# Optimization experiments

Hardware: AMD Instinct MI355X
Metric: run time of the kernel (lower is better)

The kernel has to match this reference:

```python
import jax, jax.numpy as jnp
import numpy as np

IN_DIM = 256
OUT_DIM = 256
EMBED_DIM = 256
GROUPS = 8
BN_EPS = 1e-5


def conv2d(x, w, b, pad, groups=1):
    # x: NCHW, w: OIHW (I = in_ch / groups)
    out = jax.lax.conv_general_dilated(
        x, w, window_strides=(1, 1), padding=[(pad, pad), (pad, pad)],
        dimension_numbers=('NCHW', 'OIHW', 'NCHW'), feature_group_count=groups)
    return out + b[None, :, None, None]


def setup_inputs() -> dict:
    key = jax.random.key(0)
    ks = jax.random.split(key, 8)
    s = 0.05
    d = {}
    d['x'] = jax.random.normal(ks[0], (2, IN_DIM, 16, 16), jnp.float32)
    d['y'] = jax.random.normal(ks[1], (2, OUT_DIM, 128, 128), jnp.float32)
    # channle_reduce: Conv2d(256, 64, k=3, groups=64) -> weight (64, 4, 3, 3)
    d['w_cr'] = jax.random.normal(ks[2], (IN_DIM // 4, 4, 3, 3), jnp.float32) * s
    d['b_cr'] = jnp.zeros((IN_DIM // 4,), jnp.float32)
    # depthwise convs on 64 channels
    d['w_dw3'] = jax.random.normal(ks[3], (IN_DIM // 4, 1, 3, 3), jnp.float32) * s
    d['b_dw3'] = jnp.zeros((IN_DIM // 4,), jnp.float32)
    d['w_dw7'] = jax.random.normal(ks[4], (IN_DIM // 4, 1, 5, 5), jnp.float32) * s
    d['b_dw7'] = jnp.zeros((IN_DIM // 4,), jnp.float32)
    # gate: Conv2d(256, 128, 1) + BN + StarReLU
    d['w_gate'] = jax.random.normal(ks[5], (IN_DIM // 2, IN_DIM, 1, 1), jnp.float32) * s
    d['b_gate'] = jnp.zeros((IN_DIM // 2,), jnp.float32)
    d['bn_gamma'] = jnp.ones((IN_DIM // 2,), jnp.float32)
    d['bn_beta'] = jnp.zeros((IN_DIM // 2,), jnp.float32)
    d['bn_mean'] = jnp.zeros((IN_DIM // 2,), jnp.float32)
    d['bn_var'] = jnp.ones((IN_DIM // 2,), jnp.float32)
    d['sr_scale'] = jnp.ones((1,), jnp.float32)
    d['sr_bias'] = jnp.zeros((1,), jnp.float32)
    # linear1: Linear(16, 8192) -> torch weight shape (8192, 16)
    d['w_lin'] = jax.random.normal(ks[6], (OUT_DIM * EMBED_DIM // GROUPS, IN_DIM // (2 * GROUPS)), jnp.float32) * s
    d['b_lin'] = jnp.zeros((OUT_DIM * EMBED_DIM // GROUPS,), jnp.float32)
    return d


def reference(x, y, w_cr, b_cr, w_dw3, b_dw3, w_dw7, b_dw7, w_gate, b_gate,
              bn_gamma, bn_beta, bn_mean, bn_var, sr_scale, sr_bias, w_lin, b_lin):
    B, C, H, Wd = x.shape
    # gate branch: 1x1 conv -> BN (inference stats) -> StarReLU
    g = conv2d(x, w_gate, b_gate, 0)
    inv = (bn_gamma / jnp.sqrt(bn_var + BN_EPS))[None, :, None, None]
    g = (g - bn_mean[None, :, None, None]) * inv + bn_beta[None, :, None, None]
    g = sr_scale * jnp.square(jnp.maximum(g, 0.0)) + sr_bias
    # feature branch
    xr = conv2d(x, w_cr, b_cr, 1, groups=IN_DIM // 4)        # (B, 64, H, W)
    x3 = conv2d(xr, w_dw3, b_dw3, 1, groups=IN_DIM // 4)
    x7 = conv2d(xr, w_dw7, b_dw7, 2, groups=IN_DIM // 4)
    xc = jnp.concatenate([x3, x7], axis=1) * g               # (B, 128, H, W)
    # per-pixel weight generation: (B,H,W,G,16) @ (16,8192)
    xc = xc.reshape(B, GROUPS, -1, H, Wd).transpose(0, 3, 4, 1, 2)
    wdec = jnp.einsum('bhwgi,oi->bhwgo', xc, w_lin) + b_lin  # (B,H,W,8,8192)
    # flatten (G, out*embed/G) -> (embed, out); matches torch reshape order
    wdec = wdec.reshape(B, H, Wd, EMBED_DIM, OUT_DIM)
    # patch-wise dynamic 1x1 conv == per-patch batched matmul
    b, c, h, w = y.shape
    fh, fw = H, Wd
    ph, pw = h // fh, w // fw
    yp = y.reshape(b, c, fh, ph, fw, pw)
    # out[b,e,f,p,g,q] = sum_c wdec[b,f,g,e,c] * y[b,c,f,p,g,q]
    out = jnp.einsum('bfgec,bcfpgq->befpgq', wdec, yp)
    return out.reshape(b, EMBED_DIM, h, w)
```

## Files before the change

kernel.cpp:

```cpp
#include <hip/hip_runtime.h>
#include <stdint.h>


typedef __attribute__((ext_vector_type(8))) short short8;
typedef __attribute__((ext_vector_type(4))) float f32x4;

#define BN_EPS 1e-5f

__device__ __forceinline__ unsigned short f2bf(float f) {
  unsigned u = __float_as_uint(f);
  return (unsigned short)((u + 0x8000u) >> 16);
}
__device__ __forceinline__ unsigned pk2bf(float a, float b) {
  unsigned ua = __float_as_uint(a), ub = __float_as_uint(b);
  return ((ua + 0x8000u) >> 16) | ((ub + 0x8000u) & 0xFFFF0000u);
}

__global__ __launch_bounds__(256) void k1a_groupconv(
    const float* __restrict__ x, const float* __restrict__ w_cr,
    const float* __restrict__ b_cr, float* __restrict__ xr)
{
  __shared__ float xs[4][256];
  int b = blockIdx.x >> 6, cr = blockIdx.x & 63;
  int t = threadIdx.x;
  {
    int ch = t >> 6, off = (t & 63) * 4;
    float4 v = *(const float4*)(x + b * 65536 + (cr * 4 + ch) * 256 + off);
    *(float4*)&xs[ch][off] = v;
  }
  __syncthreads();
  int h = t >> 4, w = t & 15;
  float a = b_cr[cr];
  #pragma unroll
  for (int ii = 0; ii < 4; ++ii) {
    const float* wp = w_cr + (cr * 4 + ii) * 9;
    #pragma unroll
    for (int ky = 0; ky < 3; ++ky) {
      int gy = h + ky - 1;
      #pragma unroll
      for (int kx = 0; kx < 3; ++kx) {
        int gx = w + kx - 1;
        float v = (gy >= 0 && gy < 16 && gx >= 0 && gx < 16) ? xs[ii][gy * 16 + gx] : 0.f;
        a += wp[ky * 3 + kx] * v;
      }
    }
  }
  xr[(b * 64 + cr) * 256 + t] = a;
}

__global__ __launch_bounds__(256) void k1b_gate_dw(
    const float* __restrict__ x, const float* __restrict__ xr,
    const float* __restrict__ w_dw3, const float* __restrict__ b_dw3,
    const float* __restrict__ w_dw7, const float* __restrict__ b_dw7,
    const float* __restrict__ w_gate, const float* __restrict__ b_gate,
    const float* __restrict__ bn_gamma, const float* __restrict__ bn_beta,
    const float* __restrict__ bn_mean, const float* __restrict__ bn_var,
    const float* __restrict__ sr_scale, const float* __restrict__ sr_bias,
    const float* __restrict__ w_lin, short* __restrict__ wlin_bf, short* __restrict__ xc_bf)
{
  __shared__ float xcen[256];
  __shared__ float gs[128];
  int blk = blockIdx.x;
  int b = blk >> 8, h = (blk >> 4) & 15, w = blk & 15;
  int t = threadIdx.x;

  { int idx = blk * 256 + t; wlin_bf[idx] = (short)f2bf(w_lin[idx]); }

  xcen[t] = x[b * 65536 + t * 256 + h * 16 + w];
  __syncthreads();

  int o = t >> 1, half = t & 1;
  {
    const float* wrow = w_gate + o * 256 + half * 128;
    const float* xcn  = xcen + half * 128;
    float ga = 0.f;
    #pragma unroll 8
    for (int ci = 0; ci < 128; ci += 4) {
      float4 wv = *(const float4*)(wrow + ci);
      float4 xv = *(const float4*)(xcn + ci);
      ga += wv.x * xv.x + wv.y * xv.y + wv.z * xv.z + wv.w * xv.w;
    }
    ga += __shfl_xor(ga, 1);
    float inv = bn_gamma[o] * rsqrtf(bn_var[o] + BN_EPS);
    float gg = (ga + b_gate[o] - bn_mean[o]) * inv + bn_beta[o];
    gg = fmaxf(gg, 0.f);
    gg = sr_scale[0] * gg * gg + sr_bias[0];
    if (half == 0) gs[o] = gg;
  }
  __syncthreads();

  if (t < 128) {
    int oc = t;
    float f0;
    if (oc < 64) {
      f0 = b_dw3[oc];
      const float* wp = w_dw3 + oc * 9;
      const float* xp = xr + (b * 64 + oc) * 256;
      #pragma unroll
      for (int ky = 0; ky < 3; ++ky) {
        int gy = h + ky - 1;
        #pragma unroll
        for (int kx = 0; kx < 3; ++kx) {
          int gx = w + kx - 1;
          float v = (gy >= 0 && gy < 16 && gx >= 0 && gx < 16) ? xp[gy * 16 + gx] : 0.f;
          f0 += wp[ky * 3 + kx] * v;
        }
      }
    } else {
      int c5 = oc - 64;
      f0 = b_dw7[c5];
      const float* wp = w_dw7 + c5 * 25;
      const float* xp = xr + (b * 64 + c5) * 256;
      #pragma unroll
      for (int ky = 0; ky < 5; ++ky) {
        int gy = h + ky - 2;
        #pragma unroll
        for (int kx = 0; kx < 5; ++kx) {
          int gx = w + kx - 2;
          float v = (gy >= 0 && gy < 16 && gx >= 0 && gx < 16) ? xp[gy * 16 + gx] : 0.f;
          f0 += wp[ky * 5 + kx] * v;
        }
      }
    }
    int pix = (b * 16 + h) * 16 + w;
    xc_bf[pix * 128 + oc] = (short)f2bf(f0 * gs[oc]);
  }
}

__global__ __launch_bounds__(256) void k2a_wgen(
    const short* __restrict__ wlin_bf, const short* __restrict__ xc_bf,
    const float* __restrict__ b_lin, short* __restrict__ wd)
{
  __shared__ __align__(16) short Wt[16 * 2048];
  int blk = blockIdx.x;
  int n0 = (blk >> 2) * 16;
  int oc = (blk & 3) * 2048;
  int tid = threadIdx.x;
  int wave = tid >> 6, lane = tid & 63;
  int quad = lane >> 4, l16 = lane & 15;

  short8 af = {0, 0, 0, 0, 0, 0, 0, 0};
  if (quad < 2) af = *(const short8*)(xc_bf + (n0 + l16) * 16 + quad * 8);

  f32x4 zero4 = {0.f, 0.f, 0.f, 0.f};
  #pragma unroll 8
  for (int i = 0; i < 32; ++i) {
    int o0 = wave * 512 + i * 16;
    short8 bf = {0, 0, 0, 0, 0, 0, 0, 0};
    if (quad < 2) bf = *(const short8*)(wlin_bf + (oc + o0 + l16) * 16 + quad * 8);
    f32x4 d = __builtin_amdgcn_mfma_f32_16x16x32_bf16(af, bf, zero4, 0, 0, 0);
    float bl = b_lin[oc + o0 + l16];
    #pragma unroll
    for (int r = 0; r < 4; ++r)
      Wt[(quad * 4 + r) * 2048 + o0 + l16] = (short)f2bf(d[r] + bl);
  }
  __syncthreads();

  const uint2* src = (const uint2*)Wt;
  #pragma unroll 8
  for (int j = 0; j < 32; ++j) {
    int fl = j * 256 + tid;
    int row = fl >> 9;
    int col = (fl & 511) * 4;
    *(uint2*)(wd + (size_t)(n0 + row) * 8192 + oc + col) = src[fl];
  }
}

__global__ __launch_bounds__(512, 6) void k2b_dynconv(
    const float* __restrict__ y, const short* __restrict__ wd,
    float* __restrict__ out)
{
  __shared__ __align__(16) short Ylds[8192];
  __shared__ __align__(16) float scratch[4096];

  int phys = blockIdx.x;
  int x_ = phys & 7, q_ = phys >> 3;
  int sub = q_ & 3, pphi = q_ >> 2;
  int pp = pphi * 8 + x_;
  int b = pp >> 7, f = (pp >> 3) & 15, gp = pp & 7;
  int g = gp * 2 + (sub & 1);
  int half = sub >> 1;

  int tid = threadIdx.x;
  int wave = tid >> 6, lane = tid & 63;
  int quad = lane >> 4, l16 = lane & 15;

  const float* yb = y + b * 4194304 + (f * 8 + half * 4) * 128 + g * 8;
  const short* wdp = wd + (size_t)(((b * 16 + f) * 16 + g)) * 65536;

  for (int pass = 0; pass < 2; ++pass) {
    #pragma unroll
    for (int it = 0; it < 2; ++it) {
      int task = it * 512 + tid;
      int c = task >> 3, pf = task & 7;
      float4 v = *(const float4*)(yb + (pass * 128 + c) * 16384 + (pf >> 1) * 128 + (pf & 3 & 1) * 4);
      *(float4*)&scratch[c * 32 + pf * 4] = v;
    }
    __syncthreads();
    {
      int pix = tid & 31, cg = tid >> 5;
      float s0 = scratch[(cg * 8 + 0) * 32 + pix];
      float s1 = scratch[(cg * 8 + 1) * 32 + pix];
      float s2 = scratch[(cg * 8 + 2) * 32 + pix];
      float s3 = scratch[(cg * 8 + 3) * 32 + pix];
      float s4 = scratch[(cg * 8 + 4) * 32 + pix];
      float s5 = scratch[(cg * 8 + 5) * 32 + pix];
      float s6 = scratch[(cg * 8 + 6) * 32 + pix];
      float s7 = scratch[(cg * 8 + 7) * 32 + pix];
      uint4 pk;
      pk.x = pk2bf(s0, s1); pk.y = pk2bf(s2, s3);
      pk.z = pk2bf(s4, s5); pk.w = pk2bf(s6, s7);
      int chunk = pass * 16 + cg;
      int physc = chunk ^ (pix & 7);
      *(uint4*)&Ylds[pix * 256 + physc * 8] = pk;
    }
    __syncthreads();
  }

  f32x4 acc[2][2];
  f32x4 zero4 = {0.f, 0.f, 0.f, 0.f};
  #pragma unroll
  for (int et = 0; et < 2; ++et)
    #pragma unroll
    for (int nt = 0; nt < 2; ++nt)
      acc[et][nt] = zero4;

  #pragma unroll 2
  for (int cc = 0; cc < 8; ++cc) {
    short8 A[2], Bf[2];
    #pragma unroll
    for (int et = 0; et < 2; ++et) {
      int e = wave * 32 + et * 16 + l16;
      A[et] = *(const short8*)(wdp + e * 256 + cc * 32 + quad * 8);
    }
    int chunk = cc * 4 + quad;
    #pragma unroll
    for (int nt = 0; nt < 2; ++nt) {
      int nn = nt * 16 + l16;
      int physc = chunk ^ (nn & 7);
      Bf[nt] = *(const short8*)&Ylds[nn * 256 + physc * 8];
    }
    #pragma unroll
    for (int et = 0; et < 2; ++et)
      #pragma unroll
      for (int nt = 0; nt < 2; ++nt)
        acc[et][nt] = __builtin_amdgcn_mfma_f32_16x16x32_bf16(A[et], Bf[nt], acc[et][nt], 0, 0, 0);
  }

  float* ob = out + b * 4194304 + (f * 8 + half * 4) * 128 + g * 8;
  #pragma unroll
  for (int et = 0; et < 2; ++et) {
    int e0 = wave * 32 + et * 16 + quad * 4;
    #pragma unroll
    for (int nt = 0; nt < 2; ++nt) {
      int pix = nt * 16 + l16;
      float* oa = ob + (pix >> 3) * 128 + (pix & 7);
      #pragma unroll
      for (int r = 0; r < 4; ++r)
        oa[(e0 + r) * 16384] = acc[et][nt][r];
    }
  }
}

extern "C" void kernel_launch(void* const* d_in, const int* in_sizes, int n_in,
                              void* d_out, int out_size, void* d_ws, size_t ws_size,
                              hipStream_t stream) {
  const float* x        = (const float*)d_in[0];
  const float* y        = (const float*)d_in[1];
  const float* w_cr     = (const float*)d_in[2];
  const float* b_cr     = (const float*)d_in[3];
  const float* w_dw3    = (const float*)d_in[4];
  const float* b_dw3    = (const float*)d_in[5];
  const float* w_dw7    = (const float*)d_in[6];
  const float* b_dw7    = (const float*)d_in[7];
  const float* w_gate   = (const float*)d_in[8];
  const float* b_gate   = (const float*)d_in[9];
  const float* bn_gamma = (const float*)d_in[10];
  const float* bn_beta  = (const float*)d_in[11];
  const float* bn_mean  = (const float*)d_in[12];
  const float* bn_var   = (const float*)d_in[13];
  const float* sr_scale = (const float*)d_in[14];
  const float* sr_bias  = (const float*)d_in[15];
  const float* w_lin    = (const float*)d_in[16];
  const float* b_lin    = (const float*)d_in[17];
  float* out = (float*)d_out;

  short* xc_bf   = (short*)d_ws;
  short* wlin_bf = (short*)((char*)d_ws + 131072);
  float* xr      = (float*)((char*)d_ws + 131072 + 262144);
  short* wd      = (short*)((char*)d_ws + 131072 + 262144 + 131072);

  hipLaunchKernelGGL(k1a_groupconv, dim3(128), dim3(256), 0, stream, x, w_cr, b_cr, xr);
  hipLaunchKernelGGL(k1b_gate_dw, dim3(512), dim3(256), 0, stream,
                     x, xr, w_dw3, b_dw3, w_dw7, b_dw7, w_gate, b_gate,
                     bn_gamma, bn_beta, bn_mean, bn_var, sr_scale, sr_bias,
                     w_lin, wlin_bf, xc_bf);
  hipLaunchKernelGGL(k2a_wgen, dim3(1024), dim3(256), 0, stream,
                     wlin_bf, xc_bf, b_lin, wd);
  hipLaunchKernelGGL(k2b_dynconv, dim3(1024), dim3(512), 0, stream, y, wd, out);
}
```

Baseline: 180.6 us.

## Fuse weight generation into dynamic conv by reassociating the per-pixel matmul

Removes the kernel that materializes the 64 MB-scale bf16 per-pixel weight tensor and instead computes W_lin^T·Y first, then contracts with the 16-wide xc vector plus a bias term via a second small MFMA. w_lin is transposed to bf16 and b_lin converted in the first kernel. This eliminates the large global write and read of generated weights at the cost of more MFMA work per block (wlinT re-read from L2 per block) and an extra bf16 rounding of the intermediate.

```diff
diff --git a/kernel.cpp b/kernel.cpp
--- a/kernel.cpp
+++ b/kernel.cpp
@@ -56,7 +56,8 @@
     const float* __restrict__ bn_gamma, const float* __restrict__ bn_beta,
     const float* __restrict__ bn_mean, const float* __restrict__ bn_var,
     const float* __restrict__ sr_scale, const float* __restrict__ sr_bias,
-    const float* __restrict__ w_lin, short* __restrict__ wlin_bf, short* __restrict__ xc_bf)
+    const float* __restrict__ w_lin, const float* __restrict__ b_lin,
+    short* __restrict__ wlinT, short* __restrict__ blin_bf, short* __restrict__ xc_bf)
 {
   __shared__ float xcen[256];
   __shared__ float gs[128];
@@ -64,7 +65,14 @@
   int b = blk >> 8, h = (blk >> 4) & 15, w = blk & 15;
   int t = threadIdx.x;
 
-  { int idx = blk * 256 + t; wlin_bf[idx] = (short)f2bf(w_lin[idx]); }
+  {
+    int idx = blk * 256 + t;
+    wlinT[(idx & 15) * 8192 + (idx >> 4)] = (short)f2bf(w_lin[idx]);
+  }
+  if (blk < 32) {
+    int idx = blk * 256 + t;
+    blin_bf[idx] = (short)f2bf(b_lin[idx]);
+  }
 
   xcen[t] = x[b * 65536 + t * 256 + h * 16 + w];
   __syncthreads();
@@ -127,47 +135,9 @@
   }
 }
 
-__global__ __launch_bounds__(256) void k2a_wgen(
-    const short* __restrict__ wlin_bf, const short* __restrict__ xc_bf,
-    const float* __restrict__ b_lin, short* __restrict__ wd)
-{
-  __shared__ __align__(16) short Wt[16 * 2048];
-  int blk = blockIdx.x;
-  int n0 = (blk >> 2) * 16;
-  int oc = (blk & 3) * 2048;
-  int tid = threadIdx.x;
-  int wave = tid >> 6, lane = tid & 63;
-  int quad = lane >> 4, l16 = lane & 15;
-
-  short8 af = {0, 0, 0, 0, 0, 0, 0, 0};
-  if (quad < 2) af = *(const short8*)(xc_bf + (n0 + l16) * 16 + quad * 8);
-
-  f32x4 zero4 = {0.f, 0.f, 0.f, 0.f};
-  #pragma unroll 8
-  for (int i = 0; i < 32; ++i) {
-    int o0 = wave * 512 + i * 16;
-    short8 bf = {0, 0, 0, 0, 0, 0, 0, 0};
-    if (quad < 2) bf = *(const short8*)(wlin_bf + (oc + o0 + l16) * 16 + quad * 8);
-    f32x4 d = __builtin_amdgcn_mfma_f32_16x16x32_bf16(af, bf, zero4, 0, 0, 0);
-    float bl = b_lin[oc + o0 + l16];
-    #pragma unroll
-    for (int r = 0; r < 4; ++r)
-      Wt[(quad * 4 + r) * 2048 + o0 + l16] = (short)f2bf(d[r] + bl);
-  }
-  __syncthreads();
-
-  const uint2* src = (const uint2*)Wt;
-  #pragma unroll 8
-  for (int j = 0; j < 32; ++j) {
-    int fl = j * 256 + tid;
-    int row = fl >> 9;
-    int col = (fl & 511) * 4;
-    *(uint2*)(wd + (size_t)(n0 + row) * 8192 + oc + col) = src[fl];
-  }
-}
-
-__global__ __launch_bounds__(512, 6) void k2b_dynconv(
-    const float* __restrict__ y, const short* __restrict__ wd,
+__global__ __launch_bounds__(256, 4) void k2_fused(
+    const float* __restrict__ y, const short* __restrict__ wlinT,
+    const short* __restrict__ blin, const short* __restrict__ xc_bf,
     float* __restrict__ out)
 {
   __shared__ __align__(16) short Ylds[8192];
@@ -184,21 +154,24 @@
   int tid = threadIdx.x;
   int wave = tid >> 6, lane = tid & 63;
   int quad = lane >> 4, l16 = lane & 15;
+  int pt = wave & 1, jh = wave >> 1;
+  int npix = (b * 16 + f) * 16 + g;
 
   const float* yb = y + b * 4194304 + (f * 8 + half * 4) * 128 + g * 8;
-  const short* wdp = wd + (size_t)(((b * 16 + f) * 16 + g)) * 65536;
 
   for (int pass = 0; pass < 2; ++pass) {
     #pragma unroll
+    for (int it = 0; it < 4; ++it) {
+      int task = it * 256 + tid;
+      int c = task >> 3, pf = task & 7;
+      *(float4*)&scratch[c * 32 + pf * 4] =
+          *(const float4*)(yb + (pass * 128 + c) * 16384 + (pf >> 1) * 128 + (pf & 1) * 4);
+    }
+    __syncthreads();
+    #pragma unroll
     for (int it = 0; it < 2; ++it) {
-      int task = it * 512 + tid;
-      int c = task >> 3, pf = task & 7;
-      float4 v = *(const float4*)(yb + (pass * 128 + c) * 16384 + (pf >> 1) * 128 + (pf & 3 & 1) * 4);
-      *(float4*)&scratch[c * 32 + pf * 4] = v;
-    }
-    __syncthreads();
-    {
-      int pix = tid & 31, cg = tid >> 5;
+      int task = it * 256 + tid;
+      int pix = task & 31, cg = task >> 5;
       float s0 = scratch[(cg * 8 + 0) * 32 + pix];
       float s1 = scratch[(cg * 8 + 1) * 32 + pix];
       float s2 = scratch[(cg * 8 + 2) * 32 + pix];
@@ -211,53 +184,72 @@
       pk.x = pk2bf(s0, s1); pk.y = pk2bf(s2, s3);
       pk.z = pk2bf(s4, s5); pk.w = pk2bf(s6, s7);
       int chunk = pass * 16 + cg;
-      int physc = chunk ^ (pix & 7);
-      *(uint4*)&Ylds[pix * 256 + physc * 8] = pk;
+      int ph = chunk ^ (pix & 7);
+      *(uint4*)&Ylds[pix * 256 + ph * 8] = pk;
     }
     __syncthreads();
   }
 
-  f32x4 acc[2][2];
+  short8 Bh[8];
+  int nn = pt * 16 + l16;
+  #pragma unroll
+  for (int kc = 0; kc < 8; ++kc) {
+    int chunk = kc * 4 + quad;
+    int ph = chunk ^ (nn & 7);
+    Bh[kc] = *(const short8*)&Ylds[nn * 256 + ph * 8];
+  }
+
+  short* tw = (short*)scratch + wave * 1024;
   f32x4 zero4 = {0.f, 0.f, 0.f, 0.f};
-  #pragma unroll
-  for (int et = 0; et < 2; ++et)
-    #pragma unroll
-    for (int nt = 0; nt < 2; ++nt)
-      acc[et][nt] = zero4;
+
+  {
+    f32x4 du = zero4;
+    #pragma unroll
+    for (int kc = 0; kc < 8; ++kc) {
+      short8 ab = *(const short8*)(blin + (jh * 16 + l16) * 256 + kc * 32 + quad * 8);
+      du = __builtin_amdgcn_mfma_f32_16x16x32_bf16(ab, Bh[kc], du, 0, 0, 0);
+    }
+    uint2 pk; pk.x = pk2bf(du[0], du[1]); pk.y = pk2bf(du[2], du[3]);
+    *(uint2*)&tw[512 + l16 * 16 + quad * 4] = pk;
+  }
+
+  short8 a2 = {0, 0, 0, 0, 0, 0, 0, 0};
+  if (quad < 2) {
+    if (l16 < 8) a2 = *(const short8*)(xc_bf + npix * 128 + l16 * 16 + quad * 8);
+  } else if (quad == 2) {
+    a2[0] = (short)0x3F80;
+  }
+
+  float* ob = out + b * 4194304 + (f * 8 + half * 4) * 128 + g * 8;
+  int pix = pt * 16 + l16;
+  float* oa = ob + (pix >> 3) * 128 + (pix & 7);
 
   #pragma unroll 2
-  for (int cc = 0; cc < 8; ++cc) {
-    short8 A[2], Bf[2];
-    #pragma unroll
-    for (int et = 0; et < 2; ++et) {
-      int e = wave * 32 + et * 16 + l16;
-      A[et] = *(const short8*)(wdp + e * 256 + cc * 32 + quad * 8);
-    }
-    int chunk = cc * 4 + quad;
-    #pragma unroll
-    for (int nt = 0; nt < 2; ++nt) {
-      int nn = nt * 16 + l16;
-      int physc = chunk ^ (nn & 7);
-      Bf[nt] = *(const short8*)&Ylds[nn * 256 + physc * 8];
-    }
-    #pragma unroll
-    for (int et = 0; et < 2; ++et)
-      #pragma unroll
-      for (int nt = 0; nt < 2; ++nt)
-        acc[et][nt] = __builtin_amdgcn_mfma_f32_16x16x32_bf16(A[et], Bf[nt], acc[et][nt], 0, 0, 0);
-  }
-
-  float* ob = out + b * 4194304 + (f * 8 + half * 4) * 128 + g * 8;
-  #pragma unroll
-  for (int et = 0; et < 2; ++et) {
-    int e0 = wave * 32 + et * 16 + quad * 4;
-    #pragma unroll
-    for (int nt = 0; nt < 2; ++nt) {
-      int pix = nt * 16 + l16;
-      float* oa = ob + (pix >> 3) * 128 + (pix & 7);
+  for (int j = 0; j < 16; ++j) {
+    int jg = jh * 16 + j;
+    const short* ap = wlinT + l16 * 8192 + jg * 256 + quad * 8;
+    f32x4 d = zero4;
+    #pragma unroll
+    for (int kc = 0; kc < 8; ++kc) {
+      short8 af = *(const short8*)(ap + kc * 32);
+      d = __builtin_amdgcn_mfma_f32_16x16x32_bf16(af, Bh[kc], d, 0, 0, 0);
+    }
+    short* tb = tw + (j & 1) * 256;
+    {
+      uint2 pk; pk.x = pk2bf(d[0], d[1]); pk.y = pk2bf(d[2], d[3]);
+      *(uint2*)&tb[l16 * 16 + quad * 4] = pk;
+    }
+    short8 b2 = {0, 0, 0, 0, 0, 0, 0, 0};
+    if (quad < 2) {
+      b2 = *(const short8*)&tb[l16 * 16 + quad * 8];
+    } else if (quad == 2) {
+      b2[0] = tw[512 + l16 * 16 + j];
+    }
+    f32x4 d2 = __builtin_amdgcn_mfma_f32_16x16x32_bf16(a2, b2, zero4, 0, 0, 0);
+    if (quad < 2) {
       #pragma unroll
       for (int r = 0; r < 4; ++r)
-        oa[(e0 + r) * 16384] = acc[et][nt][r];
+        oa[(size_t)((quad * 4 + r) * 32 + jg) * 16384] = d2[r];
     }
   }
 }
@@ -286,16 +278,15 @@
   float* out = (float*)d_out;
 
   short* xc_bf   = (short*)d_ws;
-  short* wlin_bf = (short*)((char*)d_ws + 131072);
-  float* xr      = (float*)((char*)d_ws + 131072 + 262144);
-  short* wd      = (short*)((char*)d_ws + 131072 + 262144 + 131072);
+  short* wlinT   = (short*)((char*)d_ws + 131072);
+  short* blin_bf = (short*)((char*)d_ws + 131072 + 262144);
+  float* xr      = (float*)((char*)d_ws + 131072 + 262144 + 16384);
 
   hipLaunchKernelGGL(k1a_groupconv, dim3(128), dim3(256), 0, stream, x, w_cr, b_cr, xr);
   hipLaunchKernelGGL(k1b_gate_dw, dim3(512), dim3(256), 0, stream,
                      x, xr, w_dw3, b_dw3, w_dw7, b_dw7, w_gate, b_gate,
                      bn_gamma, bn_beta, bn_mean, bn_var, sr_scale, sr_bias,
-                     w_lin, wlin_bf, xc_bf);
-  hipLaunchKernelGGL(k2a_wgen, dim3(1024), dim3(256), 0, stream,
-                     wlin_bf, xc_bf, b_lin, wd);
-  hipLaunchKernelGGL(k2b_dynconv, dim3(1024), dim3(512), 0, stream, y, wd, out);
-}
+                     w_lin, b_lin, wlinT, blin_bf, xc_bf);
+  hipLaunchKernelGGL(k2_fused, dim3(1024), dim3(256), 0, stream,
+                     y, wlinT, blin_bf, xc_bf, out);
+}
```

Measured after the change: 194.4 us. 7.6% more time.
